# Performance work log

Hardware: AMD Instinct MI355X
Metric: run time of the kernel (lower is better)

Reference implementation:

```python
import jax, jax.numpy as jnp
import numpy as np

O, EI, EQ = 1024, 512, 512      # output_size, embedding_img, embedding_q
DI, DQ = 2048, 300              # input_img, input_q
LI, LQ = 1024, 32               # video frames, question length
V, T = 32000, 20                # vocab, decode steps


def _lstm_scan(x, Wi, Wh, b):
    # x: [L, D]; torch LSTM gate order i, f, g, o
    xp = x @ Wi.T  # [L, 4H] precompute input projection
    H = Wh.shape[1]
    def step(carry, xt):
        h, c = carry
        g = xt + Wh @ h + b
        i, f, gg, o = jnp.split(g, 4)
        c = jax.nn.sigmoid(f) * c + jax.nn.sigmoid(i) * jnp.tanh(gg)
        h = jax.nn.sigmoid(o) * jnp.tanh(c)
        return (h, c), h
    z = jnp.zeros((H,), x.dtype)
    _, hs = jax.lax.scan(step, (z, z), xp)
    return hs  # [L, H]


def _bilstm(x, Wif, Whf, bf, Wib, Whb, bb):
    hf = _lstm_scan(x, Wif, Whf, bf)
    hb = _lstm_scan(x[::-1], Wib, Whb, bb)[::-1]
    return jnp.concatenate([hf, hb], axis=-1)  # [L, 2H]


def _forward(img_feats, q_feats, Wi_imgf, Wh_imgf, b_imgf, Wi_imgb, Wh_imgb, b_imgb, Wi_qf, Wh_qf, b_qf, Wi_qb, Wh_qb, b_qb, Wimg_h, Wimg_e, bimg, Wq_h, Wq_e, bq, Wmod, bmod, Wmod_img, Wmod_q, Wfus_img, Wfus_q, Wfus, bfus, Wi_dec, Wh_dec, b_dec, Wfin, bfin, t_dec):
    img_emb = _bilstm(img_feats, Wi_imgf, Wh_imgf, b_imgf, Wi_imgb, Wh_imgb, b_imgb)  # [LI, 2EI]
    q_emb = _bilstm(q_feats, Wi_qf, Wh_qf, b_qf, Wi_qb, Wh_qb, b_qb)                  # [LQ, 2EQ]
    # static (encoder) part of the Bahdanau score: Linear(O+2E,1) split into h-part and e-part
    e_img = img_emb @ Wimg_e + bimg  # [LI]
    e_q = q_emb @ Wq_e + bq          # [LQ]

    def dec_step(carry, _):
        h, c = carry  # decoder hidden/cell, [O]
        # per-frame / per-word attention (h contribution is a constant shift under softmax)
        a_img = jax.nn.softmax(jnp.dot(Wimg_h, h) + e_img)
        a_q = jax.nn.softmax(jnp.dot(Wq_h, h) + e_q)
        ctx_img = a_img @ img_emb  # [2EI]
        ctx_q = a_q @ q_emb        # [2EQ]
        # modality-level attention
        tmp = jnp.dot(Wmod, h) + bmod
        wi = jnp.tanh(tmp + jnp.dot(Wmod_img, ctx_img))
        wq = jnp.tanh(tmp + jnp.dot(Wmod_q, ctx_q))
        mw = jax.nn.softmax(jnp.stack([wi, wq]))  # [2]
        d_img = Wfus_img @ ctx_img  # [O]
        d_q = Wfus_q @ ctx_q        # [O]
        fs = jnp.tanh(Wfus @ h + bfus + mw[0] * d_img + mw[1] * d_q)  # gated fusion, [O]
        # single-step decoder LSTM
        g = Wi_dec @ fs + Wh_dec @ h + b_dec
        i, f, gg, o = jnp.split(g, 4)
        c = jax.nn.sigmoid(f) * c + jax.nn.sigmoid(i) * jnp.tanh(gg)
        h = jax.nn.sigmoid(o) * jnp.tanh(c)
        logits = Wfin @ h + bfin  # [V]
        return (h, c), logits

    z = jnp.zeros((O,), img_feats.dtype)
    _, logits = jax.lax.scan(dec_step, (z, z), None, length=t_dec)
    return logits  # [T, V]


def setup_inputs() -> dict:
    ks = jax.random.split(jax.random.key(0), 40)
    def n(k, shape, s=0.05):
        return jax.random.normal(k, shape, dtype=jnp.float32) * s
    inp = {
        "img_feats": n(ks[0], (LI, DI), 1.0),
        "q_feats": n(ks[1], (LQ, DQ), 1.0),
        "Wi_imgf": n(ks[2], (4 * EI, DI)),
        "Wh_imgf": n(ks[3], (4 * EI, EI)),
        "b_imgf": n(ks[4], (4 * EI,)),
        "Wi_imgb": n(ks[5], (4 * EI, DI)),
        "Wh_imgb": n(ks[6], (4 * EI, EI)),
        "b_imgb": n(ks[7], (4 * EI,)),
        "Wi_qf": n(ks[8], (4 * EQ, DQ)),
        "Wh_qf": n(ks[9], (4 * EQ, EQ)),
        "b_qf": n(ks[10], (4 * EQ,)),
        "Wi_qb": n(ks[11], (4 * EQ, DQ)),
        "Wh_qb": n(ks[12], (4 * EQ, EQ)),
        "b_qb": n(ks[13], (4 * EQ,)),
        "Wimg_h": n(ks[14], (O,)),
        "Wimg_e": n(ks[15], (2 * EI,)),
        "bimg": n(ks[16], ()),
        "Wq_h": n(ks[17], (O,)),
        "Wq_e": n(ks[18], (2 * EQ,)),
        "bq": n(ks[19], ()),
        "Wmod": n(ks[20], (O,)),
        "bmod": n(ks[21], ()),
        "Wmod_img": n(ks[22], (2 * EI,)),
        "Wmod_q": n(ks[23], (2 * EQ,)),
        "Wfus_img": n(ks[24], (O, 2 * EI)),
        "Wfus_q": n(ks[25], (O, 2 * EQ)),
        "Wfus": n(ks[26], (O, O)),
        "bfus": n(ks[27], (O,)),
        "Wi_dec": n(ks[28], (4 * O, O)),
        "Wh_dec": n(ks[29], (4 * O, O)),
        "b_dec": n(ks[30], (4 * O,)),
        "Wfin": n(ks[31], (V, O)),
        "bfin": n(ks[32], (V,)),
        "t_dec": T,
    }
    return inp


def reference(img_feats, q_feats, Wi_imgf, Wh_imgf, b_imgf, Wi_imgb, Wh_imgb, b_imgb, Wi_qf, Wh_qf, b_qf, Wi_qb, Wh_qb, b_qb, Wimg_h, Wimg_e, bimg, Wq_h, Wq_e, bq, Wmod, bmod, Wmod_img, Wmod_q, Wfus_img, Wfus_q, Wfus, bfus, Wi_dec, Wh_dec, b_dec, Wfin, bfin, t_dec):
    return _forward(img_feats, q_feats, Wi_imgf, Wh_imgf, b_imgf, Wi_imgb, Wh_imgb, b_imgb, Wi_qf, Wh_qf, b_qf, Wi_qb, Wh_qb, b_qb, Wimg_h, Wimg_e, bimg, Wq_h, Wq_e, bq, Wmod, bmod, Wmod_img, Wmod_q, Wfus_img, Wfus_q, Wfus, bfus, Wi_dec, Wh_dec, b_dec, Wfin, bfin, t_dec)
```

## Files before the change

kernel.cpp:

```cpp
#include <hip/hip_runtime.h>
#include <hip/hip_bf16.h>

typedef unsigned int  u32;
typedef unsigned short u16;
typedef unsigned long long u64;
typedef float f32x4 __attribute__((ext_vector_type(4)));
typedef short bf16x8 __attribute__((ext_vector_type(8)));
typedef u32 u32x4 __attribute__((ext_vector_type(4)));

#define AGENT __HIP_MEMORY_SCOPE_AGENT
__device__ inline float aloadf(const float* p){ return __hip_atomic_load(p, __ATOMIC_RELAXED, AGENT); }
__device__ inline void  astoref(float* p, float v){ __hip_atomic_store(p, v, __ATOMIC_RELAXED, AGENT); }
__device__ inline int   aloadi(const int* p){ return __hip_atomic_load(p, __ATOMIC_RELAXED, AGENT); }
__device__ inline void  astorei_rel(int* p, int v){ __hip_atomic_store(p, v, __ATOMIC_RELEASE, AGENT); }

__device__ __host__ inline u16 f2bf(float f){
  u32 u = __builtin_bit_cast(u32, f);
  u += 0x7fffu + ((u >> 16) & 1u);
  return (u16)(u >> 16);
}
__device__ inline float bflo(u32 a){ return __uint_as_float(a << 16); }
__device__ inline float bfhi(u32 a){ return __uint_as_float(a & 0xffff0000u); }

__device__ inline float sigm(float x){
  return __builtin_amdgcn_rcpf(1.f + __expf(-x));
}
__device__ inline float ftanh(float x){
  float xc = fminf(fmaxf(x, -15.f), 15.f);
  float e = __expf(2.f * xc);
  return (e - 1.f) * __builtin_amdgcn_rcpf(e + 1.f);
}

__device__ inline u32x4 poll4(const u32* addr, u32 want){
  u32x4 w;
  do {
    asm volatile("global_load_dwordx4 %0, %1, off sc0 sc1\n\ts_waitcnt vmcnt(0)"
                 : "=&v"(w) : "v"(addr) : "memory");
  } while ((w.x >> 16) != want || (w.y >> 16) != want ||
           (w.z >> 16) != want || (w.w >> 16) != want);
  return w;
}
__device__ inline u32x4 poll4_dual(const u32* loc, const u32* glob, u32 want){
  u32x4 w;
  for (;;){
    asm volatile("global_load_dwordx4 %0, %1, off sc0\n\ts_waitcnt vmcnt(0)"
                 : "=&v"(w) : "v"(loc) : "memory");
    if ((w.x >> 16) == want && (w.y >> 16) == want &&
        (w.z >> 16) == want && (w.w >> 16) == want) return w;
    asm volatile("global_load_dwordx4 %0, %1, off sc0 sc1\n\ts_waitcnt vmcnt(0)"
                 : "=&v"(w) : "v"(glob) : "memory");
    if ((w.x >> 16) == want && (w.y >> 16) == want &&
        (w.z >> 16) == want && (w.w >> 16) == want) return w;
  }
}
__device__ inline void store4(u32* addr, u32x4 q){
  asm volatile("global_store_dwordx4 %0, %1, off sc0 sc1"
               :: "v"(addr), "v"(q) : "memory");
}
__device__ inline void store4_loc(u32* addr, u32x4 q){
  asm volatile("global_store_dwordx4 %0, %1, off sc0"
               :: "v"(addr), "v"(q) : "memory");
}

__device__ inline float wred_sum(float v){
#pragma unroll
  for (int m = 32; m >= 1; m >>= 1) v += __shfl_xor(v, m, 64);
  return v;
}
__device__ inline float bred_sum(float v, float* red, int tid){
  v = wred_sum(v);
  if ((tid & 63) == 0) red[tid >> 6] = v;
  __syncthreads();
  float r = red[0] + red[1] + red[2] + red[3];
  __syncthreads();
  return r;
}
__device__ inline float bred_max(float v, float* red, int tid){
#pragma unroll
  for (int m = 32; m >= 1; m >>= 1) v = fmaxf(v, __shfl_xor(v, m, 64));
  if ((tid & 63) == 0) red[tid >> 6] = v;
  __syncthreads();
  float r = fmaxf(fmaxf(red[0], red[1]), fmaxf(red[2], red[3]));
  __syncthreads();
  return r;
}

__device__ inline float dot1024(const u16* __restrict__ row, const float* h, int lane){
  float s = 0.f;
#pragma unroll
  for (int c = 0; c < 4; ++c){
    int e = 4 * lane + 256 * c;
    uint2 a = *(const uint2*)(row + e);
    float4 x = *(const float4*)(h + e);
    s = fmaf(bflo(a.x), x.x, s); s = fmaf(bfhi(a.x), x.y, s);
    s = fmaf(bflo(a.y), x.z, s); s = fmaf(bfhi(a.y), x.w, s);
  }
  return s;
}

__device__ inline float4 dot4(const u16* __restrict__ W, size_t r, size_t rs,
                              const float* h, int lane){
  const u16* p0 = W + (r         ) * 1024;
  const u16* p1 = W + (r + rs    ) * 1024;
  const u16* p2 = W + (r + 2 * rs) * 1024;
  const u16* p3 = W + (r + 3 * rs) * 1024;
  float s0 = 0, s1 = 0, s2 = 0, s3 = 0;
#pragma unroll
  for (int c = 0; c < 4; ++c){
    int e = 4 * lane + 256 * c;
    float4 x = *(const float4*)(h + e);
    uint2 a0 = *(const uint2*)(p0 + e);
    uint2 a1 = *(const uint2*)(p1 + e);
    uint2 a2 = *(const uint2*)(p2 + e);
    uint2 a3 = *(const uint2*)(p3 + e);
    s0 = fmaf(bflo(a0.x), x.x, s0); s0 = fmaf(bfhi(a0.x), x.y, s0);
    s0 = fmaf(bflo(a0.y), x.z, s0); s0 = fmaf(bfhi(a0.y), x.w, s0);
    s1 = fmaf(bflo(a1.x), x.x, s1); s1 = fmaf(bfhi(a1.x), x.y, s1);
    s1 = fmaf(bflo(a1.y), x.z, s1); s1 = fmaf(bfhi(a1.y), x.w, s1);
    s2 = fmaf(bflo(a2.x), x.x, s2); s2 = fmaf(bfhi(a2.x), x.y, s2);
    s2 = fmaf(bflo(a2.y), x.z, s2); s2 = fmaf(bfhi(a2.y), x.w, s2);
    s3 = fmaf(bflo(a3.x), x.x, s3); s3 = fmaf(bfhi(a3.x), x.y, s3);
    s3 = fmaf(bflo(a3.y), x.z, s3); s3 = fmaf(bfhi(a3.y), x.w, s3);
  }
  s0 = wred_sum(s0); s1 = wred_sum(s1); s2 = wred_sum(s2); s3 = wred_sum(s3);
  return make_float4(s0, s1, s2, s3);
}

__global__ void k_cvt(const float* __restrict__ s, u16* __restrict__ d, int n4){
  int i = blockIdx.x * 256 + threadIdx.x;
  int stride = gridDim.x * 256;
  const float4* s4 = (const float4*)s;
  for (; i < n4; i += stride){
    float4 v = s4[i];
    ushort4 o;
    o.x = f2bf(v.x); o.y = f2bf(v.y); o.z = f2bf(v.z); o.w = f2bf(v.w);
    ((ushort4*)d)[i] = o;
  }
}

__global__ __launch_bounds__(256, 1) void k_gemm_xp(
    const u16* __restrict__ A,
    const u16* __restrict__ B0, const u16* __restrict__ B1,
    const float* __restrict__ bias0, const float* __restrict__ bias1,
    float* __restrict__ C0, float* __restrict__ C1)
{
  const int K = 2048, N = 2048;
  const int bx = blockIdx.x, by = blockIdx.y, z = blockIdx.z;
  const u16* B = z ? B1 : B0;
  const float* bias = z ? bias1 : bias0;
  float* C = z ? C1 : C0;
  const int tid = threadIdx.x;
  const int lane = tid & 63, wv = tid >> 6;
  const int m0 = by * 128, n0 = bx * 128;
  const int wm = (wv >> 1) * 64, wn = (wv & 1) * 64;

  __shared__ __align__(16) u16 lA[128 * 32];
  __shared__ __align__(16) u16 lB[128 * 32];

  f32x4 acc[4][4];
#pragma unroll
  for (int i = 0; i < 4; ++i)
#pragma unroll
    for (int j = 0; j < 4; ++j) acc[i][j] = (f32x4){0.f, 0.f, 0.f, 0.f};

  const int lrow = tid >> 2;
  const int lcol = (tid & 3) * 8;
  const u16* aBase = A + (size_t)(m0 + lrow) * K + lcol;
  const u16* bBase = B + (size_t)(n0 + lrow) * K + lcol;

  for (int kk = 0; kk < K; kk += 32){
#pragma unroll
    for (int io = 0; io < 2; ++io){
      __builtin_amdgcn_global_load_lds(
        (const __attribute__((address_space(1))) void*)(aBase + (size_t)io * 64 * K + kk),
        (__attribute__((address_space(3))) void*)((char*)lA + wv * 1024 + io * 4096), 16, 0, 0);
      __builtin_amdgcn_global_load_lds(
        (const __attribute__((address_space(1))) void*)(bBase + (size_t)io * 64 * K + kk),
        (__attribute__((address_space(3))) void*)((char*)lB + wv * 1024 + io * 4096), 16, 0, 0);
    }
    asm volatile("s_waitcnt vmcnt(0)");
    __syncthreads();

    bf16x8 af[4], bfr[4];
#pragma unroll
    for (int i = 0; i < 4; ++i){
      af[i]  = *(const bf16x8*)&lA[(wm + i * 16 + (lane & 15)) * 32 + (lane >> 4) * 8];
      bfr[i] = *(const bf16x8*)&lB[(wn + i * 16 + (lane & 15)) * 32 + (lane >> 4) * 8];
    }
#pragma unroll
    for (int i = 0; i < 4; ++i)
#pragma unroll
      for (int j = 0; j < 4; ++j)
        acc[i][j] = __builtin_amdgcn_mfma_f32_16x16x32_bf16(af[i], bfr[j], acc[i][j], 0, 0, 0);
    __syncthreads();
  }

  const int rbase = (lane >> 4) * 4;
  const int ccol = lane & 15;
#pragma unroll
  for (int i = 0; i < 4; ++i)
#pragma unroll
    for (int j = 0; j < 4; ++j){
      int col = n0 + wn + j * 16 + ccol;
      float bv = bias[col];
#pragma unroll
      for (int r2 = 0; r2 < 4; ++r2){
        int row = m0 + wm + i * 16 + rbase + r2;
        C[(size_t)row * N + col] = acc[i][j][r2] + bv;
      }
    }
}

__global__ __launch_bounds__(256, 1) void k_qxp(
    const float* __restrict__ qf,
    const float* __restrict__ W0, const float* __restrict__ W1,
    const float* __restrict__ bb0, const float* __restrict__ bb1,
    float* __restrict__ o0, float* __restrict__ o1)
{
  const int bx = blockIdx.x;
  const int z = blockIdx.y;
  const float* W = z ? W1 : W0;
  const float* bb = z ? bb1 : bb0;
  float* o = z ? o1 : o0;
  const int tid = threadIdx.x;
  __shared__ float xs[32 * 301];
  __shared__ float Ws[64 * 301];
  for (int idx = tid; idx < 32 * 300; idx += 256){
    int m = idx / 300, k = idx - m * 300;
    xs[m * 301 + k] = qf[idx];
  }
  for (int idx = tid; idx < 64 * 300; idx += 256){
    int j = idx / 300, k = idx - j * 300;
    Ws[j * 301 + k] = W[(size_t)(bx * 64 + j) * 300 + k];
  }
  __syncthreads();
  for (int i = 0; i < 8; ++i){
    int idx = tid + i * 256;
    int nl = idx >> 5, m = idx & 31;
    float s = 0;
    for (int k = 0; k < 300; ++k) s = fmaf(xs[m * 301 + k], Ws[nl * 301 + k], s);
    o[(size_t)m * 2048 + bx * 64 + nl] = s + bb[bx * 64 + nl];
  }
}

__global__ __launch_bounds__(256, 1) void k_scan(
    const float* __restrict__ WhA, const float* __restrict__ WhB,
    const float* __restrict__ WhC, const float* __restrict__ WhD,
    const float* __restrict__ xpA, const float* __restrict__ xpB,
    const float* __restrict__ xpC, const float* __restrict__ xpD,
    float* __restrict__ emb, float* __restrict__ embT,
    float* __restrict__ qemb, float* __restrict__ qembT,
    u32* hcommL, u32* hcommG )
{
  const int b = blockIdx.x;
  const int slot = b & 7;
  if (slot >= 4) return;
  const int dir = slot;
  const int sub = b >> 3;
  const int tid = threadIdx.x;
  const float* Wh = dir == 0 ? WhA : dir == 1 ? WhB : dir == 2 ? WhC : WhD;
  const float* xp = dir == 0 ? xpA : dir == 1 ? xpB : dir == 2 ? xpC : xpD;
  const int L = (dir < 2) ? 1024 : 32;
  const int rev = dir & 1;
  float* oe  = (dir < 2) ? emb  : qemb;
  float* oeT = (dir < 2) ? embT : qembT;
  const int colbase = rev ? 512 : 0;
  const int eTL = (dir < 2) ? 1024 : 32;
  const int hbase = sub * 16;
  const int lane = tid & 63, wv = tid >> 6;
  const int g = tid >> 4;
  const int seg = tid & 15;
  const bool pub = (seg == 0);

  __shared__ float hl[2][512];

  int grows[4];
#pragma unroll
  for (int gate = 0; gate < 4; ++gate) grows[gate] = gate * 512 + hbase + g;

  u32 wpk0[16], wpk1[16], wpk2[16], wpk3[16];
  {
    const float2* r0 = (const float2*)(Wh + (size_t)grows[0] * 512) + seg;
    const float2* r1 = (const float2*)(Wh + (size_t)grows[1] * 512) + seg;
    const float2* r2 = (const float2*)(Wh + (size_t)grows[2] * 512) + seg;
    const float2* r3 = (const float2*)(Wh + (size_t)grows[3] * 512) + seg;
#pragma unroll
    for (int i = 0; i < 16; ++i){
      float2 a0 = r0[16 * i], a1 = r1[16 * i], a2 = r2[16 * i], a3 = r3[16 * i];
      wpk0[i] = (u32)f2bf(a0.x) | ((u32)f2bf(a0.y) << 16);
      wpk1[i] = (u32)f2bf(a1.x) | ((u32)f2bf(a1.y) << 16);
      wpk2[i] = (u32)f2bf(a2.x) | ((u32)f2bf(a2.y) << 16);
      wpk3[i] = (u32)f2bf(a3.x) | ((u32)f2bf(a3.y) << 16);
    }
  }

  float creg = 0.f;
  float xpv[4] = {0.f, 0.f, 0.f, 0.f};
  if (pub){
    int t0 = rev ? (L - 1) : 0;
#pragma unroll
    for (int gate = 0; gate < 4; ++gate) xpv[gate] = xp[(size_t)t0 * 2048 + grows[gate]];
  }

  u32* hcl = hcommL + dir * 1024;
  u32* hcg = hcommG + dir * 1024;

  for (int t = 0; t < L; ++t){
    const u32 want = (u32)t;
    const int par = t & 1;
    if (tid < 128){
      int o = (par << 9) + 4 * tid;
      u32x4 w = poll4_dual(hcl + o, hcg + o, want);
      *(float4*)&hl[par][4 * tid] =
          make_float4(bflo(w.x), bflo(w.y), bflo(w.z), bflo(w.w));
    }
    __syncthreads();

    float2 hreg[16];
#pragma unroll
    for (int i = 0; i < 16; ++i) hreg[i] = *(const float2*)&hl[par][2 * (seg + 16 * i)];
    float s0 = 0, s1 = 0, s2 = 0, s3 = 0;
#pragma unroll
    for (int i = 0; i < 16; ++i){
      float hx = hreg[i].x, hy = hreg[i].y;
      s0 = fmaf(bflo(wpk0[i]), hx, s0); s0 = fmaf(bfhi(wpk0[i]), hy, s0);
      s1 = fmaf(bflo(wpk1[i]), hx, s1); s1 = fmaf(bfhi(wpk1[i]), hy, s1);
      s2 = fmaf(bflo(wpk2[i]), hx, s2); s2 = fmaf(bfhi(wpk2[i]), hy, s2);
      s3 = fmaf(bflo(wpk3[i]), hx, s3); s3 = fmaf(bfhi(wpk3[i]), hy, s3);
    }
#pragma unroll
    for (int m = 1; m < 16; m <<= 1){
      s0 += __shfl_xor(s0, m, 64); s1 += __shfl_xor(s1, m, 64);
      s2 += __shfl_xor(s2, m, 64); s3 += __shfl_xor(s3, m, 64);
    }
    u32 tg = 0;
    float hout = 0.f;
    if (pub){
      float gi = s0 + xpv[0], gf = s1 + xpv[1], gg = s2 + xpv[2], go = s3 + xpv[3];
      creg = sigm(gf) * creg + sigm(gi) * ftanh(gg);
      hout = sigm(go) * ftanh(creg);
      tg = ((u32)(t + 1) << 16) | (u32)f2bf(hout);
    }
    u32 q0 = __shfl(tg, 0), q1 = __shfl(tg, 16), q2 = __shfl(tg, 32), q3 = __shfl(tg, 48);
    if (lane == 0){
      int o = (((t + 1) & 1) << 9) + hbase + 4 * wv;
      u32x4 q = {q0, q1, q2, q3};
      store4_loc(hcl + o, q);
      store4(hcg + o, q);
    }
    if (pub){
      const int trow = rev ? (L - 1 - t) : t;
      int col = colbase + hbase + g;
      oe[(size_t)trow * 1024 + col] = hout;
      oeT[(size_t)col * eTL + trow] = hout;
      if (t + 1 < L){
        int tn = rev ? (L - 2 - t) : (t + 1);
#pragma unroll
        for (int gate = 0; gate < 4; ++gate) xpv[gate] = xp[(size_t)tn * 2048 + grows[gate]];
      }
    }
  }
}

#define DG 64
__device__ inline void dbar(int* st, int b, int pc, int tid){
  __syncthreads();
  if (tid == 0) astorei_rel(&st[b], pc);
  if (tid < DG){
    while (aloadi(&st[tid]) < pc) {}
  }
  __syncthreads();
}

struct DecArgs {
  const float *emb, *embT, *qemb, *qembT;
  const float *Wimg_e, *bimg, *Wmod_img;
  const float *Wq_e, *bq, *Wmod_q;
  const float *Wmod, *bmod;
  const u16 *Wfus_bf; const float *bfus;
  const u16 *WfusI_bf, *WfusQ_bf;
  const u16 *Wid_bf, *Whd_bf; const float *b_dec;
  float *e_img, *m_img, *e_q, *m_q;
  float *a_img, *a_q, *ctx_img, *ctx_q;
  float *d_img, *d_q, *scal;
  u32 *tfs, *thdec;
  float *hall;
  int *st; int T;
};

__global__ __launch_bounds__(256, 1) void k_dec(DecArgs A)
{
  const int b = blockIdx.x, tid = threadIdx.x;
  const int lane = tid & 63, wv = tid >> 6;
  __shared__ __align__(16) float hl[1024];
  __shared__ __align__(16) float fsl[1024];
  __shared__ float red[4];
  __shared__ float gb[4][16];
  __shared__ float cdec[16];
  __shared__ float aql[32];
  int pc = 0;

  {
#pragma unroll
    for (int rr = 0; rr < 4; ++rr){
      int l = b * 16 + wv * 4 + rr;
      const float* er = A.emb + (size_t)l * 1024;
      float se = 0, sm = 0;
#pragma unroll
      for (int i = 0; i < 16; ++i){
        int k = lane + (i << 6);
        float x = er[k];
        se = fmaf(x, A.Wimg_e[k], se);
        sm = fmaf(x, A.Wmod_img[k], sm);
      }
      se = wred_sum(se); sm = wred_sum(sm);
      if (lane == 0){ astoref(A.e_img + l, se + A.bimg[0]); astoref(A.m_img + l, sm); }
    }
    if (b < 32 && wv == 0){
      const float* qr = A.qemb + (size_t)b * 1024;
      float se2 = 0, sm2 = 0;
#pragma unroll
      for (int i = 0; i < 16; ++i){
        int k = lane + (i << 6);
        float x = qr[k];
        se2 = fmaf(x, A.Wq_e[k], se2);
        sm2 = fmaf(x, A.Wmod_q[k], sm2);
      }
      se2 = wred_sum(se2); sm2 = wred_sum(sm2);
      if (lane == 0){ astoref(A.e_q + b, se2 + A.bq[0]); astoref(A.m_q + b, sm2); }
    }
  }
  pc++; dbar(A.st, b, pc, tid);

  if (b == 0){
    for (int k = tid; k < 1024; k += 256){ fsl[k] = aloadf(A.e_img + k); hl[k] = aloadf(A.m_img + k); }
    __syncthreads();
    float lm = -3.4e38f;
    for (int k = tid; k < 1024; k += 256) lm = fmaxf(lm, fsl[k]);
    float M = bred_max(lm, red, tid);
    float ls = 0, lw = 0;
    for (int k = tid; k < 1024; k += 256){
      float e = expf(fsl[k] - M);
      fsl[k] = e; ls += e; lw += e * hl[k];
    }
    float S = bred_sum(ls, red, tid);
    float W = bred_sum(lw, red, tid);
    float inv = 1.f / S;
    for (int k = tid; k < 1024; k += 256) astoref(A.a_img + k, fsl[k] * inv);
    if (tid == 0) astoref(A.scal + 2, W * inv);
    if (tid < 64){
      float ev = (lane < 32) ? aloadf(A.e_q + lane) : -3.4e38f;
      float mv = (lane < 32) ? aloadf(A.m_q + lane) : 0.f;
      float M2 = ev;
#pragma unroll
      for (int m = 32; m >= 1; m >>= 1) M2 = fmaxf(M2, __shfl_xor(M2, m, 64));
      float e = (lane < 32) ? expf(ev - M2) : 0.f;
      float S2 = wred_sum(e);
      float W2 = wred_sum(e * mv);
      if (lane < 32) astoref(A.a_q + lane, e / S2);
      if (lane == 0) astoref(A.scal + 3, W2 / S2);
    }
  }
  pc++; dbar(A.st, b, pc, tid);

  {
    for (int k = tid; k < 1024; k += 256) hl[k] = aloadf(A.a_img + k);
    if (tid < 32) aql[tid] = aloadf(A.a_q + tid);
    __syncthreads();
#pragma unroll
    for (int cc = 0; cc < 4; ++cc){
      int c = b * 16 + wv * 4 + cc;
      const float* eT = A.embT + (size_t)c * 1024;
      float s = 0;
#pragma unroll
      for (int i = 0; i < 16; ++i){ int l = lane + (i << 6); s = fmaf(hl[l], eT[l], s); }
      s = wred_sum(s);
      if (lane == 0) astoref(A.ctx_img + c, s);
      const float* qT = A.qembT + (size_t)c * 32;
      float sq = (lane < 32) ? aql[lane] * qT[lane] : 0.f;
      sq = wred_sum(sq);
      if (lane == 0) astoref(A.ctx_q + c, sq);
    }
  }
  pc++; dbar(A.st, b, pc, tid);

  for (int k = tid; k < 1024; k += 256){ hl[k] = aloadf(A.ctx_img + k); fsl[k] = aloadf(A.ctx_q + k); }
  __syncthreads();
  {
    int r = b * 16 + wv * 4;
    float4 si = dot4(A.WfusI_bf, (size_t)r, 1, hl, lane);
    float4 sq = dot4(A.WfusQ_bf, (size_t)r, 1, fsl, lane);
    if (lane == 0){
      astoref(A.d_img + r + 0, si.x); astoref(A.d_q + r + 0, sq.x);
      astoref(A.d_img + r + 1, si.y); astoref(A.d_q + r + 1, sq.y);
      astoref(A.d_img + r + 2, si.z); astoref(A.d_q + r + 2, sq.z);
      astoref(A.d_img + r + 3, si.w); astoref(A.d_q + r + 3, sq.w);
    }
  }
  pc++; dbar(A.st, b, pc, tid);

  const int fr = b * 16 + wv * 4;
  float dimg_r[4], dq_r[4], bfus_r[4];
#pragma unroll
  for (int rr = 0; rr < 4; ++rr){
    dimg_r[rr] = aloadf(A.d_img + fr + rr);
    dq_r[rr]   = aloadf(A.d_q + fr + rr);
    bfus_r[rr] = A.bfus[fr + rr];
  }
  const float sc2 = aloadf(A.scal + 2), sc3 = aloadf(A.scal + 3);
  const float bmod0 = A.bmod[0];
  float wmod_r[4];
#pragma unroll
  for (int i = 0; i < 4; ++i) wmod_r[i] = A.Wmod[tid + (i << 8)];

  for (int k = tid; k < 1024; k += 256) hl[k] = 0.f;
  if (tid < 16) cdec[tid] = 0.f;
  __syncthreads();

  for (int t = 0; t < A.T; ++t){
    const u32 want = (u32)(t + 1);

    float part = 0;
#pragma unroll
    for (int i = 0; i < 4; ++i) part = fmaf(wmod_r[i], hl[tid + (i << 8)], part);
    float tmp = bred_sum(part, red, tid) + bmod0;
    float wi_ = ftanh(tmp + sc2), wq_ = ftanh(tmp + sc3);
    float mx = fmaxf(wi_, wq_);
    float e0 = __expf(wi_ - mx), e1 = __expf(wq_ - mx);
    float inv01 = __builtin_amdgcn_rcpf(e0 + e1);
    float mw0 = e0 * inv01, mw1 = e1 * inv01;

    {
      float4 sf = dot4(A.Wfus_bf, (size_t)fr, 1, hl, lane);
      if (lane == 0){
        float v0 = ftanh(sf.x + bfus_r[0] + mw0 * dimg_r[0] + mw1 * dq_r[0]);
        float v1 = ftanh(sf.y + bfus_r[1] + mw0 * dimg_r[1] + mw1 * dq_r[1]);
        float v2 = ftanh(sf.z + bfus_r[2] + mw0 * dimg_r[2] + mw1 * dq_r[2]);
        float v3 = ftanh(sf.w + bfus_r[3] + mw0 * dimg_r[3] + mw1 * dq_r[3]);
        u32x4 q = { (want << 16) | (u32)f2bf(v0), (want << 16) | (u32)f2bf(v1),
                    (want << 16) | (u32)f2bf(v2), (want << 16) | (u32)f2bf(v3) };
        store4(A.tfs + fr, q);
      }
    }

    const size_t g0 = (size_t)wv * 1024 + b * 16;
    float4 sbq[4];
#pragma unroll
    for (int q4 = 0; q4 < 4; ++q4)
      sbq[q4] = dot4(A.Whd_bf, g0 + q4 * 4, 1, hl, lane);

    {
      u32x4 w = poll4(A.tfs + 4 * tid, want);
      *(float4*)&fsl[4 * tid] = make_float4(bflo(w.x), bflo(w.y), bflo(w.z), bflo(w.w));
    }
    __syncthreads();

    {
#pragma unroll
      for (int q4 = 0; q4 < 4; ++q4){
        float4 sa = dot4(A.Wid_bf, g0 + q4 * 4, 1, fsl, lane);
        if (lane == 0){
          gb[wv][q4 * 4 + 0] = sa.x + sbq[q4].x + A.b_dec[g0 + q4 * 4 + 0];
          gb[wv][q4 * 4 + 1] = sa.y + sbq[q4].y + A.b_dec[g0 + q4 * 4 + 1];
          gb[wv][q4 * 4 + 2] = sa.z + sbq[q4].z + A.b_dec[g0 + q4 * 4 + 2];
          gb[wv][q4 * 4 + 3] = sa.w + sbq[q4].w + A.b_dec[g0 + q4 * 4 + 3];
        }
      }
    }
    __syncthreads();
    u32 tg = 0;
    if (tid < 16){
      float gi = gb[0][tid], gf = gb[1][tid], gg = gb[2][tid], go = gb[3][tid];
      float c = sigm(gf) * cdec[tid] + sigm(gi) * ftanh(gg);
      cdec[tid] = c;
      float h = sigm(go) * ftanh(c);
      tg = (want << 16) | (u32)f2bf(h);
      A.hall[(size_t)t * 1024 + b * 16 + tid] = h;
    }
    if (wv == 0){
      u32 q0 = __shfl(tg, 4 * lane + 0), q1 = __shfl(tg, 4 * lane + 1);
      u32 q2 = __shfl(tg, 4 * lane + 2), q3 = __shfl(tg, 4 * lane + 3);
      if (lane < 4) store4(A.thdec + b * 16 + 4 * lane, (u32x4){q0, q1, q2, q3});
    }
    {
      u32x4 w = poll4(A.thdec + 4 * tid, want);
      *(float4*)&hl[4 * tid] = make_float4(bflo(w.x), bflo(w.y), bflo(w.z), bflo(w.w));
    }
    __syncthreads();
  }
}

__global__ __launch_bounds__(256, 1) void k_logits(
    const u16* __restrict__ Wfin, const float* __restrict__ bfin,
    const float* __restrict__ hall, float* __restrict__ out, int T)
{
  __shared__ u32 hp[20 * 512];
  const int tid = threadIdx.x;
  const int lane = tid & 63, wv = tid >> 6;
  const int n2 = T * 512;
  for (int idx = tid; idx < n2; idx += 256){
    float2 v = ((const float2*)hall)[idx];
    hp[idx] = (u32)f2bf(v.x) | ((u32)f2bf(v.y) << 16);
  }
  __syncthreads();
  const int gwv = blockIdx.x * 4 + wv;
#pragma unroll
  for (int gset = 0; gset < 4; ++gset){
    int r0 = gwv * 16 + gset * 4;
    uint2 wreg[4][4];
#pragma unroll
    for (int rr = 0; rr < 4; ++rr){
      const uint2* wr = (const uint2*)(Wfin + (size_t)(r0 + rr) * 1024);
#pragma unroll
      for (int c = 0; c < 4; ++c) wreg[rr][c] = wr[lane + 64 * c];
    }
    for (int t = 0; t < T; ++t){
      const uint2* hp2 = (const uint2*)&hp[t * 512];
      float s0 = 0, s1 = 0, s2 = 0, s3 = 0;
#pragma unroll
      for (int c = 0; c < 4; ++c){
        uint2 hw = hp2[lane + 64 * c];
        float h0 = bflo(hw.x), h1 = bfhi(hw.x), h2 = bflo(hw.y), h3 = bfhi(hw.y);
        uint2 a;
        a = wreg[0][c];
        s0 = fmaf(bflo(a.x), h0, s0); s0 = fmaf(bfhi(a.x), h1, s0);
        s0 = fmaf(bflo(a.y), h2, s0); s0 = fmaf(bfhi(a.y), h3, s0);
        a = wreg[1][c];
        s1 = fmaf(bflo(a.x), h0, s1); s1 = fmaf(bfhi(a.x), h1, s1);
        s1 = fmaf(bflo(a.y), h2, s1); s1 = fmaf(bfhi(a.y), h3, s1);
        a = wreg[2][c];
        s2 = fmaf(bflo(a.x), h0, s2); s2 = fmaf(bfhi(a.x), h1, s2);
        s2 = fmaf(bflo(a.y), h2, s2); s2 = fmaf(bfhi(a.y), h3, s2);
        a = wreg[3][c];
        s3 = fmaf(bflo(a.x), h0, s3); s3 = fmaf(bfhi(a.x), h1, s3);
        s3 = fmaf(bflo(a.y), h2, s3); s3 = fmaf(bfhi(a.y), h3, s3);
      }
      s0 = wred_sum(s0); s1 = wred_sum(s1); s2 = wred_sum(s2); s3 = wred_sum(s3);
      if (lane == 0){
        float* orow = out + (size_t)t * 32000;
        orow[r0 + 0] = s0 + bfin[r0 + 0];
        orow[r0 + 1] = s1 + bfin[r0 + 1];
        orow[r0 + 2] = s2 + bfin[r0 + 2];
        orow[r0 + 3] = s3 + bfin[r0 + 3];
      }
    }
  }
}

extern "C" void kernel_launch(void* const* d_in, const int* in_sizes, int n_in,
                              void* d_out, int out_size, void* d_ws, size_t ws_size,
                              hipStream_t stream)
{
  const float* img_feats = (const float*)d_in[0];
  const float* q_feats   = (const float*)d_in[1];
  const float* Wi_imgf = (const float*)d_in[2];
  const float* Wh_imgf = (const float*)d_in[3];
  const float* b_imgf  = (const float*)d_in[4];
  const float* Wi_imgb = (const float*)d_in[5];
  const float* Wh_imgb = (const float*)d_in[6];
  const float* b_imgb  = (const float*)d_in[7];
  const float* Wi_qf = (const float*)d_in[8];
  const float* Wh_qf = (const float*)d_in[9];
  const float* b_qf  = (const float*)d_in[10];
  const float* Wi_qb = (const float*)d_in[11];
  const float* Wh_qb = (const float*)d_in[12];
  const float* b_qb  = (const float*)d_in[13];
  const float* Wimg_e = (const float*)d_in[15];
  const float* bimg   = (const float*)d_in[16];
  const float* Wq_e   = (const float*)d_in[18];
  const float* bq     = (const float*)d_in[19];
  const float* Wmod   = (const float*)d_in[20];
  const float* bmod   = (const float*)d_in[21];
  const float* Wmod_img = (const float*)d_in[22];
  const float* Wmod_q   = (const float*)d_in[23];
  const float* Wfus_img = (const float*)d_in[24];
  const float* Wfus_q   = (const float*)d_in[25];
  const float* Wfus     = (const float*)d_in[26];
  const float* bfus     = (const float*)d_in[27];
  const float* Wi_dec = (const float*)d_in[28];
  const float* Wh_dec = (const float*)d_in[29];
  const float* b_dec  = (const float*)d_in[30];
  const float* Wfin = (const float*)d_in[31];
  const float* bfin = (const float*)d_in[32];
  const int T = out_size / 32000;

  char* ws = (char*)d_ws;
  size_t off = 0;
  auto alloc = [&](size_t bytes){ size_t o = off; off += (bytes + 255) & ~(size_t)255; return o; };
  const size_t oA    = alloc(1024ull * 2048 * 2);
  const size_t oWiF  = alloc(2048ull * 2048 * 2);
  const size_t oWiB  = alloc(2048ull * 2048 * 2);
  const size_t oWfin = alloc(32000ull * 1024 * 2);
  const size_t oWfu  = alloc(1024ull * 1024 * 2);
  const size_t oWfI  = alloc(1024ull * 1024 * 2);
  const size_t oWfQ  = alloc(1024ull * 1024 * 2);
  const size_t oWid  = alloc(4096ull * 1024 * 2);
  const size_t oWhd  = alloc(4096ull * 1024 * 2);
  const size_t oxpF  = alloc(1024ull * 2048 * 4);
  const size_t oxpB  = alloc(1024ull * 2048 * 4);
  const size_t oxpQF = alloc(32ull * 2048 * 4);
  const size_t oxpQB = alloc(32ull * 2048 * 4);
  const size_t oemb  = alloc(1024ull * 1024 * 4);
  const size_t oembT = alloc(1024ull * 1024 * 4);
  const size_t oqemb = alloc(32ull * 1024 * 4);
  const size_t oqembT= alloc(1024ull * 32 * 4);
  const size_t ohall = alloc(20ull * 1024 * 4);
  const size_t oeimg = alloc(1024 * 4);
  const size_t omimg = alloc(1024 * 4);
  const size_t oeq   = alloc(32 * 4);
  const size_t omq   = alloc(32 * 4);
  const size_t oaimg = alloc(1024 * 4);
  const size_t oaq   = alloc(32 * 4);
  const size_t octxi = alloc(1024 * 4);
  const size_t octxq = alloc(1024 * 4);
  const size_t odimg = alloc(1024 * 4);
  const size_t odq   = alloc(1024 * 4);
  const size_t oCTRL = off;
  const size_t ohcommL = alloc(4ull * 2 * 512 * 4);
  const size_t ohcommG = alloc(4ull * 2 * 512 * 4);
  const size_t otfs   = alloc(1024 * 4);
  const size_t othdec = alloc(1024 * 4);
  const size_t odst   = alloc(64 * 4);
  const size_t oscal  = alloc(64 * 4);
  const size_t ctrlBytes = off - oCTRL;
  (void)ws_size; (void)n_in; (void)in_sizes;

  hipMemsetAsync(ws + oCTRL, 0, ctrlBytes, stream);

  auto cvt = [&](const float* s, size_t o, long n){
    int n4 = (int)(n >> 2);
    int g = (n4 + 255) / 256; if (g > 2048) g = 2048;
    k_cvt<<<dim3(g), dim3(256), 0, stream>>>(s, (u16*)(ws + o), n4);
  };
  cvt(img_feats, oA, 1024L * 2048);
  cvt(Wi_imgf, oWiF, 2048L * 2048);
  cvt(Wi_imgb, oWiB, 2048L * 2048);
  cvt(Wfin, oWfin, 32000L * 1024);
  cvt(Wfus, oWfu, 1024L * 1024);
  cvt(Wfus_img, oWfI, 1024L * 1024);
  cvt(Wfus_q, oWfQ, 1024L * 1024);
  cvt(Wi_dec, oWid, 4096L * 1024);
  cvt(Wh_dec, oWhd, 4096L * 1024);

  k_gemm_xp<<<dim3(16, 8, 2), dim3(256), 0, stream>>>(
      (const u16*)(ws + oA), (const u16*)(ws + oWiF), (const u16*)(ws + oWiB),
      b_imgf, b_imgb, (float*)(ws + oxpF), (float*)(ws + oxpB));

  k_qxp<<<dim3(32, 2), dim3(256), 0, stream>>>(
      q_feats, Wi_qf, Wi_qb, b_qf, b_qb,
      (float*)(ws + oxpQF), (float*)(ws + oxpQB));

  k_scan<<<dim3(256), dim3(256), 0, stream>>>(
      Wh_imgf, Wh_imgb, Wh_qf, Wh_qb,
      (const float*)(ws + oxpF), (const float*)(ws + oxpB),
      (const float*)(ws + oxpQF), (const float*)(ws + oxpQB),
      (float*)(ws + oemb), (float*)(ws + oembT),
      (float*)(ws + oqemb), (float*)(ws + oqembT),
      (u32*)(ws + ohcommL), (u32*)(ws + ohcommG));

  DecArgs DA;
  DA.emb = (const float*)(ws + oemb); DA.embT = (const float*)(ws + oembT);
  DA.qemb = (const float*)(ws + oqemb); DA.qembT = (const float*)(ws + oqembT);
  DA.Wimg_e = Wimg_e; DA.bimg = bimg; DA.Wmod_img = Wmod_img;
  DA.Wq_e = Wq_e; DA.bq = bq; DA.Wmod_q = Wmod_q;
  DA.Wmod = Wmod; DA.bmod = bmod;
  DA.Wfus_bf = (const u16*)(ws + oWfu); DA.bfus = bfus;
  DA.WfusI_bf = (const u16*)(ws + oWfI); DA.WfusQ_bf = (const u16*)(ws + oWfQ);
  DA.Wid_bf = (const u16*)(ws + oWid); DA.Whd_bf = (const u16*)(ws + oWhd); DA.b_dec = b_dec;
  DA.e_img = (float*)(ws + oeimg); DA.m_img = (float*)(ws + omimg);
  DA.e_q = (float*)(ws + oeq); DA.m_q = (float*)(ws + omq);
  DA.a_img = (float*)(ws + oaimg); DA.a_q = (float*)(ws + oaq);
  DA.ctx_img = (float*)(ws + octxi); DA.ctx_q = (float*)(ws + octxq);
  DA.d_img = (float*)(ws + odimg); DA.d_q = (float*)(ws + odq);
  DA.scal = (float*)(ws + oscal);
  DA.tfs = (u32*)(ws + otfs); DA.thdec = (u32*)(ws + othdec);
  DA.hall = (float*)(ws + ohall);
  DA.st = (int*)(ws + odst); DA.T = T;

  k_dec<<<dim3(DG), dim3(256), 0, stream>>>(DA);

  k_logits<<<dim3(500), dim3(256), 0, stream>>>(
      (const u16*)(ws + oWfin), bfin, (const float*)(ws + ohall),
      (float*)d_out, T);
}
```

Baseline: 2.059 ms.

## Claim scan roles by XCC id so each direction's blocks share one XCD

The recurrent scan kernel now reads each block's hardware XCC id and uses atomic counters to assign direction/sub-slice roles, so all 32 blocks of one LSTM direction land on the same XCD. Blocks on other XCDs fall back to claiming leftover slots, and the grid is doubled so enough blocks land on each XCD. The local poll also retries twice before checking the global copy. The intent is to cut per-step hidden-state exchange latency by keeping communication within one XCD's L2. The cost is extra idle blocks, an atomic claim protocol, and a dependence on block-to-XCD placement.

```diff
diff --git a/kernel.cpp b/kernel.cpp
--- a/kernel.cpp
+++ b/kernel.cpp
@@ -43,10 +43,13 @@
 __device__ inline u32x4 poll4_dual(const u32* loc, const u32* glob, u32 want){
   u32x4 w;
   for (;;){
-    asm volatile("global_load_dwordx4 %0, %1, off sc0\n\ts_waitcnt vmcnt(0)"
-                 : "=&v"(w) : "v"(loc) : "memory");
-    if ((w.x >> 16) == want && (w.y >> 16) == want &&
-        (w.z >> 16) == want && (w.w >> 16) == want) return w;
+#pragma unroll 1
+    for (int r = 0; r < 2; ++r){
+      asm volatile("global_load_dwordx4 %0, %1, off sc0\n\ts_waitcnt vmcnt(0)"
+                   : "=&v"(w) : "v"(loc) : "memory");
+      if ((w.x >> 16) == want && (w.y >> 16) == want &&
+          (w.z >> 16) == want && (w.w >> 16) == want) return w;
+    }
     asm volatile("global_load_dwordx4 %0, %1, off sc0 sc1\n\ts_waitcnt vmcnt(0)"
                  : "=&v"(w) : "v"(glob) : "memory");
     if ((w.x >> 16) == want && (w.y >> 16) == want &&
@@ -250,14 +253,43 @@
     const float* __restrict__ xpC, const float* __restrict__ xpD,
     float* __restrict__ emb, float* __restrict__ embT,
     float* __restrict__ qemb, float* __restrict__ qembT,
-    u32* hcommL, u32* hcommG )
+    u32* hcommL, u32* hcommG , int* claim )
 {
-  const int b = blockIdx.x;
-  const int slot = b & 7;
-  if (slot >= 4) return;
-  const int dir = slot;
-  const int sub = b >> 3;
   const int tid = threadIdx.x;
+  __shared__ int roleS[2];
+  if (tid == 0){
+    u32 xcc = 0;
+    asm volatile("s_getreg_b32 %0, hwreg(HW_REG_XCC_ID)" : "=s"(xcc));
+    int d = -1, s = 0;
+    if (xcc < 4u){
+      int t = __hip_atomic_fetch_add(&claim[xcc], 1, __ATOMIC_RELAXED, AGENT);
+      if (t < 32){ d = (int)xcc; s = t; }
+    }
+    if (d < 0){
+      for (int it = 0; it < 600; ++it){
+        if (aloadi(&claim[0]) >= 32 && aloadi(&claim[1]) >= 32 &&
+            aloadi(&claim[2]) >= 32 && aloadi(&claim[3]) >= 32) break;
+        __builtin_amdgcn_s_sleep(2);
+      }
+      for (;;){
+        bool any = false;
+        for (int q = 0; q < 4; ++q){
+          if (aloadi(&claim[q]) < 32){
+            any = true;
+            int t = __hip_atomic_fetch_add(&claim[q], 1, __ATOMIC_RELAXED, AGENT);
+            if (t < 32){ d = q; s = t; break; }
+          }
+        }
+        if (d >= 0 || !any) break;
+      }
+    }
+    roleS[0] = d; roleS[1] = s;
+  }
+  __syncthreads();
+  const int dir = roleS[0];
+  const int sub = roleS[1];
+  if (dir < 0) return;
+
   const float* Wh = dir == 0 ? WhA : dir == 1 ? WhB : dir == 2 ? WhC : WhD;
   const float* xp = dir == 0 ? xpA : dir == 1 ? xpB : dir == 2 ? xpC : xpD;
   const int L = (dir < 2) ? 1024 : 32;
@@ -335,6 +367,7 @@
     }
     u32 tg = 0;
     float hout = 0.f;
+    const int onext = (((t + 1) & 1) << 9);
     if (pub){
       float gi = s0 + xpv[0], gf = s1 + xpv[1], gg = s2 + xpv[2], go = s3 + xpv[3];
       creg = sigm(gf) * creg + sigm(gi) * ftanh(gg);
@@ -343,7 +376,7 @@
     }
     u32 q0 = __shfl(tg, 0), q1 = __shfl(tg, 16), q2 = __shfl(tg, 32), q3 = __shfl(tg, 48);
     if (lane == 0){
-      int o = (((t + 1) & 1) << 9) + hbase + 4 * wv;
+      int o = onext + hbase + 4 * wv;
       u32x4 q = {q0, q1, q2, q3};
       store4_loc(hcl + o, q);
       store4(hcg + o, q);
@@ -722,6 +755,7 @@
   const size_t othdec = alloc(1024 * 4);
   const size_t odst   = alloc(64 * 4);
   const size_t oscal  = alloc(64 * 4);
+  const size_t oclaim = alloc(16 * 4);
   const size_t ctrlBytes = off - oCTRL;
   (void)ws_size; (void)n_in; (void)in_sizes;
 
@@ -750,13 +784,13 @@
       q_feats, Wi_qf, Wi_qb, b_qf, b_qb,
       (float*)(ws + oxpQF), (float*)(ws + oxpQB));
 
-  k_scan<<<dim3(256), dim3(256), 0, stream>>>(
+  k_scan<<<dim3(512), dim3(256), 0, stream>>>(
       Wh_imgf, Wh_imgb, Wh_qf, Wh_qb,
       (const float*)(ws + oxpF), (const float*)(ws + oxpB),
       (const float*)(ws + oxpQF), (const float*)(ws + oxpQB),
       (float*)(ws + oemb), (float*)(ws + oembT),
       (float*)(ws + oqemb), (float*)(ws + oqembT),
-      (u32*)(ws + ohcommL), (u32*)(ws + ohcommG));
+      (u32*)(ws + ohcommL), (u32*)(ws + ohcommG), (int*)(ws + oclaim));
 
   DecArgs DA;
   DA.emb = (const float*)(ws + oemb); DA.embT = (const float*)(ws + oembT);
```

Result: slower. 2.173 ms (+5.5%).
